# Performance work log

Measured on AMD Instinct MI355X. Metric: run time of the kernel, lower is better.

## Reference

```python
import jax, jax.numpy as jnp
import numpy as np

CH = 50        # channel
RED = 2        # reduction -> match channels = 25
KS = 3         # ksize
SM_SCALE = 10.0
SCALES = [1.0, 0.9, 0.8, 0.7, 0.6]
ESCAPE_NAN = 1e-4


def prelu(x, a):
    return jnp.where(x >= 0, x, a * x)


def conv1x1(x, w, b):
    # x: [B,Ci,H,W], w: [Co,Ci], b: [Co]
    return jnp.einsum('bihw,oi->bohw', x, w) + b[None, :, None, None]


def patches3(x):
    # extract 3x3 stride-1 SAME patches, torch-unfold (C,kh,kw) ordering
    # x: [B,C,H,W] -> [B, H*W, C, 3, 3]
    B, C, H, W = x.shape
    p = jnp.pad(x, ((0, 0), (0, 0), (1, 1), (1, 1)))
    cols = jnp.stack([p[:, :, i:i + H, j:j + W]
                      for i in range(KS) for j in range(KS)], axis=2)  # [B,C,9,H,W]
    cols = cols.reshape(B, C, KS, KS, H * W)
    return cols.transpose(0, 4, 1, 2, 3)


def setup_inputs() -> dict:
    key = jax.random.key(0)
    ks = jax.random.split(key, 7)
    B, H, W = 4, 48, 48
    f = CH // RED  # 25
    s1 = 1.0 / np.sqrt(CH)
    return {
        'x': jax.random.normal(ks[0], (B, CH, H, W), jnp.float32),
        # conv_match_L_base: 1x1 conv CH->f + PReLU
        'w_base': jax.random.normal(ks[1], (f, CH), jnp.float32) * s1,
        'b_base': jnp.zeros((f,), jnp.float32),
        'a_base': jnp.float32(0.25),
        # conv_match: 1x1 conv CH->f + PReLU
        'w_match': jax.random.normal(ks[2], (f, CH), jnp.float32) * s1,
        'b_match': jnp.zeros((f,), jnp.float32),
        'a_match': jnp.float32(0.25),
        # conv_assembly: 1x1 conv CH->CH + PReLU
        'w_asm': jax.random.normal(ks[3], (CH, CH), jnp.float32) * s1,
        'b_asm': jnp.zeros((CH,), jnp.float32),
        'a_asm': jnp.float32(0.25),
    }


def reference(x, w_base, b_base, a_base, w_match, b_match, a_match,
              w_asm, b_asm, a_asm):
    B, C, H, W = x.shape
    match_base = prelu(conv1x1(x, w_base, b_base), a_base)  # [B,25,H,W]

    w_list, raw_list = [], []
    for s in SCALES:
        if s == 1.0:
            ref = x
        else:
            Hs, Ws = int(H * s), int(W * s)
            ref = jax.image.resize(x, (B, C, Hs, Ws), method='cubic')
        base = prelu(conv1x1(ref, w_asm, b_asm), a_asm)       # [B,C,Hs,Ws]
        raw_list.append(patches3(base))                       # [B,Hs*Ws,C,3,3]
        refm = prelu(conv1x1(ref, w_match, b_match), a_match)  # [B,25,Hs,Ws]
        w_list.append(patches3(refm))                         # [B,Hs*Ws,25,3,3]

    wi = jnp.concatenate(w_list, axis=1)    # [B, L, 25, 3, 3]
    raw = jnp.concatenate(raw_list, axis=1)  # [B, L, C, 3, 3]

    def attend(xb, wb, rb):
        # xb: [25,H,W]; wb: [L,25,3,3]; rb: [L,C,3,3]
        norm = jnp.maximum(
            jnp.sqrt(jnp.sum(wb * wb, axis=(1, 2, 3), keepdims=True)),
            ESCAPE_NAN)
        wn = wb / norm
        score = jax.lax.conv_general_dilated(
            xb[None], wn, (1, 1), [(1, 1), (1, 1)])[0]        # [L,H,W]
        attn = jax.nn.softmax(score * SM_SCALE, axis=0)
        # conv_transpose2d(stride=1, pad=1) == corr with flipped, transposed kernel
        wt = jnp.flip(rb, axis=(2, 3)).transpose(1, 0, 2, 3)  # [C,L,3,3]
        out = jax.lax.conv_general_dilated(
            attn[None], wt, (1, 1), [(1, 1), (1, 1)])[0]      # [C,H,W]
        return out * 0.25

    y = jax.vmap(attend)(match_base, wi, raw)
    return y + x  # res_scale = 1
```

## Files before the change

kernel.cpp:

```cpp
#include <hip/hip_runtime.h>
#include <hip/hip_bf16.h>
#include <hip/hip_fp16.h>
#include <math.h>


#define L_TOT 7470
#define L_PAD 7680
#define NCHUNK 4
#define CHUNK_TILES 30
#define KD    256
#define JD    512
#define HW    2304

typedef unsigned short u16;
typedef __attribute__((ext_vector_type(8))) short bf16x8;
typedef __attribute__((ext_vector_type(4))) float f32x4;

__device__ inline u16 f2b(float f) {
    __hip_bfloat16 h = __float2bfloat16(f);
    return __builtin_bit_cast(u16, h);
}
__device__ inline float b2f(u16 u) {
    __hip_bfloat16 h = __builtin_bit_cast(__hip_bfloat16, u);
    return __bfloat162float(h);
}
__device__ inline u16 f2h(float f) {
    __half h = __float2half(f);
    return __builtin_bit_cast(u16, h);
}
__device__ inline float h2f(u16 u) {
    __half h = __builtin_bit_cast(__half, u);
    return __half2float(h);
}

__constant__ int c_hs[5]   = {48, 43, 38, 33, 28};
__constant__ int c_loff[6] = {0, 2304, 4153, 5597, 6686, 7470};

#define GLOAD16(g, l) __builtin_amdgcn_global_load_lds(                          \
        (__attribute__((address_space(1))) const void*)(g),                      \
        (__attribute__((address_space(3))) void*)(l), 16, 0, 0)

__global__ void prep_kernel(float* __restrict__ wmall, int* __restrict__ dtab) {
    int r = blockIdx.x * 256 + threadIdx.x;
    if (r < 142) {
        int sizes[4] = {43, 38, 33, 28};
        int si = 0, i = r, woffs = 0;
        for (si = 0; si < 4; ++si) {
            if (i < sizes[si]) break;
            i -= sizes[si];
            woffs += sizes[si] * 48;
        }
        int osz = sizes[si];
        float inv_scale = 48.0f / (float)osz;
        float kscale = inv_scale;
        float sample_f = ((float)i + 0.5f) * inv_scale - 0.5f;
        float w[48];
        float tot = 0.f;
        for (int j = 0; j < 48; ++j) {
            float t = fabsf(sample_f - (float)j) / kscale;
            float v;
            if (t >= 2.f)       v = 0.f;
            else if (t >= 1.f)  v = ((-0.5f * t + 2.5f) * t - 4.f) * t + 2.f;
            else                v = ((1.5f * t - 2.5f) * t) * t + 1.f;
            w[j] = v;
            tot += v;
        }
        float invt = 1.f / tot;
        for (int j = 0; j < 48; ++j) wmall[woffs + i * 48 + j] = w[j] * invt;
    }
    if (r < L_PAD) {
        int v;
        if (r >= L_TOT) v = (int)0x80000000u;
        else {
            int si = 0;
#pragma unroll
            for (int s = 0; s < 4; ++s)
                if (r >= c_loff[s + 1]) si = s + 1;
            int pos = r - c_loff[si];
            int hs = c_hs[si];
            int ly = pos / hs, lx = pos % hs;
            v = si | (ly << 4) | (lx << 10);
        }
        dtab[r] = v;
    }
}

__global__ void resize_h_all(const float* __restrict__ in, const float* __restrict__ wm,
                             float* __restrict__ t1, float* __restrict__ t2,
                             float* __restrict__ t3, float* __restrict__ t4) {
    int idx = blockIdx.x * 256 + threadIdx.x;
    int rem = idx, osz, woffm;
    float* tmp;
    if (rem < 200 * 43 * 48) { osz = 43; tmp = t1; woffm = 0; }
    else {
        rem -= 200 * 43 * 48;
        if (rem < 200 * 38 * 48) { osz = 38; tmp = t2; woffm = 43 * 48; }
        else {
            rem -= 200 * 38 * 48;
            if (rem < 200 * 33 * 48) { osz = 33; tmp = t3; woffm = (43 + 38) * 48; }
            else {
                rem -= 200 * 33 * 48;
                if (rem >= 200 * 28 * 48) return;
                osz = 28; tmp = t4; woffm = (43 + 38 + 33) * 48;
            }
        }
    }
    int xi = rem % 48;
    int t = rem / 48;
    int yo = t % osz;
    int bc = t / osz;
    const float* wr = wm + (size_t)(woffm + yo * 48);
    const float* ip = in + (size_t)bc * 2304 + xi;
    float s = 0.f;
#pragma unroll
    for (int yi = 0; yi < 48; ++yi) s += wr[yi] * ip[yi * 48];
    tmp[rem] = s;
}

__global__ void resize_w_all(const float* __restrict__ t1, const float* __restrict__ t2,
                             const float* __restrict__ t3, const float* __restrict__ t4,
                             const float* __restrict__ wm,
                             float* __restrict__ r1, float* __restrict__ r2,
                             float* __restrict__ r3, float* __restrict__ r4) {
    int idx = blockIdx.x * 256 + threadIdx.x;
    int rem = idx, osz, woffm;
    const float* tmp;
    float* outp;
    if (rem < 200 * 43 * 43) { osz = 43; tmp = t1; outp = r1; woffm = 0; }
    else {
        rem -= 200 * 43 * 43;
        if (rem < 200 * 38 * 38) { osz = 38; tmp = t2; outp = r2; woffm = 43 * 48; }
        else {
            rem -= 200 * 38 * 38;
            if (rem < 200 * 33 * 33) { osz = 33; tmp = t3; outp = r3; woffm = (43 + 38) * 48; }
            else {
                rem -= 200 * 33 * 33;
                if (rem >= 200 * 28 * 28) return;
                osz = 28; tmp = t4; outp = r4; woffm = (43 + 38 + 33) * 48;
            }
        }
    }
    int xo = rem % osz;
    int t = rem / osz;
    int yo = t % osz;
    int bc = t / osz;
    const float* wr = wm + (size_t)(woffm + xo * 48);
    const float* ip = tmp + ((size_t)bc * osz + yo) * 48;
    float s = 0.f;
#pragma unroll
    for (int xi = 0; xi < 48; ++xi) s += wr[xi] * ip[xi];
    outp[rem] = s;
}

__global__ void conv_all(const float* __restrict__ x,
                         const float* __restrict__ r1, const float* __restrict__ r2,
                         const float* __restrict__ r3, const float* __restrict__ r4,
                         const float* __restrict__ w_asm, const float* __restrict__ b_asm,
                         const float* __restrict__ a_asm,
                         const float* __restrict__ w_match, const float* __restrict__ b_match,
                         const float* __restrict__ a_match,
                         const float* __restrict__ w_base, const float* __restrict__ b_base,
                         const float* __restrict__ a_base,
                         float* __restrict__ base_out, float* __restrict__ refm_out,
                         float* __restrict__ mb_out) {
    int idx = blockIdx.x * 256 + threadIdx.x;
    int rem = idx, P, loffv, NCO;
    const float* in;
    if (rem < 400 * 2304) { P = 2304; in = x; loffv = 0; NCO = 100; }
    else {
        rem -= 400 * 2304;
        if (rem < 300 * 1849) { P = 1849; in = r1; loffv = 2304; NCO = 75; }
        else {
            rem -= 300 * 1849;
            if (rem < 300 * 1444) { P = 1444; in = r2; loffv = 4153; NCO = 75; }
            else {
                rem -= 300 * 1444;
                if (rem < 300 * 1089) { P = 1089; in = r3; loffv = 5597; NCO = 75; }
                else {
                    rem -= 300 * 1089;
                    if (rem >= 300 * 784) return;
                    P = 784; in = r4; loffv = 6686; NCO = 75;
                }
            }
        }
    }
    int p = rem % P;
    int t = rem / P;
    int co = t % NCO;
    int b = t / NCO;
    const float* ip = in + (size_t)b * 50 * P + p;
    const float* wr;
    float bias, av;
    float* outp;
    if (co < 50) {
        wr = w_asm + co * 50; bias = b_asm[co]; av = a_asm[0];
        outp = base_out + (size_t)200 * loffv + ((size_t)(b * 50 + co)) * P + p;
    } else if (co < 75) {
        int cm = co - 50;
        wr = w_match + cm * 50; bias = b_match[cm]; av = a_match[0];
        outp = refm_out + (size_t)100 * loffv + ((size_t)(b * 25 + cm)) * P + p;
    } else {
        int cm = co - 75;
        wr = w_base + cm * 50; bias = b_base[cm]; av = a_base[0];
        outp = mb_out + ((size_t)(b * 25 + cm)) * P + p;
    }
    float s = bias;
#pragma unroll
    for (int ci = 0; ci < 50; ++ci) s += wr[ci] * ip[(size_t)ci * P];
    *outp = (s >= 0.f) ? s : av * s;
}

__global__ void q_build(const float* __restrict__ mb, u16* __restrict__ Q) {
    int idx = blockIdx.x * 256 + threadIdx.x;
    if (idx >= 4 * HW * 25) return;
    int c = idx % 25;
    int t = idx / 25;
    int p = t % HW;
    int b = t / HW;
    int y = p / 48, xx = p % 48;
    const float* rc = mb + (size_t)(b * 25 + c) * HW;
    u16 ov[9];
#pragma unroll
    for (int ky = 0; ky < 3; ++ky)
#pragma unroll
        for (int kx = 0; kx < 3; ++kx) {
            int yy = y + ky - 1, xv = xx + kx - 1;
            float v = (yy >= 0 && yy < 48 && xv >= 0 && xv < 48) ? rc[yy * 48 + xv] : 0.f;
            ov[ky * 3 + kx] = f2b(v);
        }
    u16* dst = Q + (size_t)(b * HW + p) * KD + c * 9;
#pragma unroll
    for (int r = 0; r < 9; ++r) dst[r] = ov[r];
    if (c == 24) {
        u16* z = dst + 9;
#pragma unroll
        for (int i = 0; i < 31; ++i) z[i] = 0;
    }
}

__global__ void norms_kernel(const float* __restrict__ refm_all, const int* __restrict__ dtab,
                             float* __restrict__ norms) {
    int idx = blockIdx.x * 256 + threadIdx.x;
    if (idx >= 4 * L_PAD) return;
    int l = idx % L_PAD;
    int b = idx / L_PAD;
    int d = dtab[l];
    if (d < 0) return;
    int si = d & 15, ly = (d >> 4) & 63, lx = (d >> 10) & 63;
    int hs = c_hs[si], P = hs * hs;
    const float* rb = refm_all + (size_t)100 * c_loff[si] + (size_t)(b * 25) * P;
    float ss = 0.f;
    for (int c = 0; c < 25; ++c) {
        const float* rc = rb + (size_t)c * P;
#pragma unroll
        for (int ky = 0; ky < 3; ++ky)
#pragma unroll
            for (int kx = 0; kx < 3; ++kx) {
                int yy = ly + ky - 1, xv = lx + kx - 1;
                if (yy >= 0 && yy < hs && xv >= 0 && xv < hs) {
                    float v = rc[yy * hs + xv];
                    ss += v * v;
                }
            }
    }
    norms[(size_t)b * L_PAD + l] = 10.0f * 1.44269504f / fmaxf(sqrtf(ss), 1e-4f);
}

__global__ void kt_build(const float* __restrict__ refm_all, const int* __restrict__ dtab,
                         const float* __restrict__ norms, u16* __restrict__ K) {
    int idx = blockIdx.x * 256 + threadIdx.x;
    if (idx >= 4 * L_PAD * 25) return;
    int c = idx % 25;
    int t = idx / 25;
    int l = t % L_PAD;
    int b = t / L_PAD;
    u16 ov[9] = {0, 0, 0, 0, 0, 0, 0, 0, 0};
    int d = dtab[l];
    if (d >= 0) {
        int si = d & 15, ly = (d >> 4) & 63, lx = (d >> 10) & 63;
        int hs = c_hs[si], P = hs * hs;
        float nrm = norms[(size_t)b * L_PAD + l];
        const float* rc = refm_all + (size_t)100 * c_loff[si] + (size_t)(b * 25 + c) * P;
#pragma unroll
        for (int ky = 0; ky < 3; ++ky)
#pragma unroll
            for (int kx = 0; kx < 3; ++kx) {
                int yy = ly + ky - 1, xv = lx + kx - 1;
                if (yy >= 0 && yy < hs && xv >= 0 && xv < hs)
                    ov[ky * 3 + kx] = f2b(rc[yy * hs + xv] * nrm);
            }
    }
    u16* dst = K + (size_t)(b * L_PAD + l) * KD + c * 9;
#pragma unroll
    for (int r = 0; r < 9; ++r) dst[r] = ov[r];
    if (c == 24) {
        u16* z = dst + 9;
#pragma unroll
        for (int i = 0; i < 31; ++i) z[i] = 0;
    }
}

__global__ void v_build(const float* __restrict__ base_all, const int* __restrict__ dtab,
                        u16* __restrict__ VT) {
    int idx = blockIdx.x * 256 + threadIdx.x;
    if (idx >= 4 * JD * (L_PAD / 8)) return;
    int l8 = idx % (L_PAD / 8);
    int t = idx / (L_PAD / 8);
    int j = t % JD;
    int b = t / JD;
    int l0 = l8 * 8;
    bf16x8 ov = (bf16x8){0, 0, 0, 0, 0, 0, 0, 0};
    if (j < 450) {
        int c = j / 9, r = j % 9, ky = r / 3, kx = r % 3;
#pragma unroll
        for (int u = 0; u < 8; ++u) {
            int d = dtab[l0 + u];
            float v = 0.f;
            if (d >= 0) {
                int si = d & 15, ly = (d >> 4) & 63, lx = (d >> 10) & 63;
                int hs = c_hs[si], P = hs * hs;
                int yy = ly + ky - 1, xv = lx + kx - 1;
                if (yy >= 0 && yy < hs && xv >= 0 && xv < hs)
                    v = base_all[(size_t)200 * c_loff[si] + (size_t)(b * 50 + c) * P + yy * hs + xv];
            }
            ov[u] = (short)f2b(v);
        }
    } else if (j == 450) {
        const u16 one = f2b(1.0f);
#pragma unroll
        for (int u = 0; u < 8; ++u)
            ov[u] = (short)(dtab[l0 + u] >= 0 ? one : 0);
    }
    *(bf16x8*)&VT[(size_t)(b * JD + j) * L_PAD + l0] = ov;
}

__global__ __launch_bounds__(256, 4) void attn_score(
    const u16* __restrict__ Qg, const u16* __restrict__ Kg,
    u16* __restrict__ SRg, float* __restrict__ mC) {
    __shared__ u16 smem[64 * KD];
    __shared__ float sm_m[2][32];
    const int bx = blockIdx.x, by = blockIdx.y;
    const int mt = by % 72, zq = by / 72;
    const int z16 = bx + 8 * zq;
    const int b = z16 >> 2, chunk = z16 & 3;
    const int bm = mt * 32;
    const u16* Q = Qg + (size_t)b * HW * KD;
    const u16* K = Kg + (size_t)b * L_PAD * KD;
    u16* SR = SRg + (size_t)b * HW * L_PAD;
    const int tid = threadIdx.x, lane = tid & 63, wid = tid >> 6;
    const int wr = wid >> 1, wc = wid & 1;
    const int l15 = lane & 15, l16 = lane >> 4, l7 = lane & 7;
    const int r_lo = lane >> 5;
    const int u_dst = lane & 31;

    {
        const u16* qrow = Q + (size_t)(bm + wid * 8 + r_lo) * KD;
        u16* qdst = smem + (size_t)(wid * 8) * KD;
#pragma unroll
        for (int q = 0; q < 4; ++q) {
            int sw = (u_dst ^ ((q * 2 + r_lo) & 7)) * 8;
            GLOAD16(qrow + (size_t)(q * 2) * KD + sw, qdst + (q * 2) * KD);
        }
    }
    __syncthreads();
    bf16x8 qf[8];
#pragma unroll
    for (int k = 0; k < 8; ++k)
        qf[k] = *(const bf16x8*)&smem[(size_t)(wr * 16 + l15) * KD + (((k * 4 + l16) ^ l7) * 8)];
    __syncthreads();

    float mrun[4] = {-3e38f, -3e38f, -3e38f, -3e38f};
    const int t0 = chunk * CHUNK_TILES;

    for (int t = t0; t < t0 + CHUNK_TILES; ++t) {
        {
            const u16* krow = K + (size_t)(t * 64 + wid * 16 + r_lo) * KD;
            u16* kdst = smem + (size_t)(wid * 16) * KD;
#pragma unroll
            for (int q = 0; q < 8; ++q) {
                int sw = (u_dst ^ ((q * 2 + r_lo) & 7)) * 8;
                GLOAD16(krow + (size_t)(q * 2) * KD + sw, kdst + (q * 2) * KD);
            }
        }
        __syncthreads();
        f32x4 acc[2];
#pragma unroll
        for (int n = 0; n < 2; ++n) acc[n] = (f32x4){0.f, 0.f, 0.f, 0.f};
#pragma unroll
        for (int k = 0; k < 8; ++k) {
            bf16x8 bfr[2];
#pragma unroll
            for (int n = 0; n < 2; ++n)
                bfr[n] = *(const bf16x8*)&smem[(size_t)(wc * 32 + n * 16 + l15) * KD
                                               + (((k * 4 + l16) ^ l7) * 8)];
#pragma unroll
            for (int n = 0; n < 2; ++n)
                acc[n] = __builtin_amdgcn_mfma_f32_16x16x32_bf16(qf[k], bfr[n], acc[n], 0, 0, 0);
        }
        const int col0 = t * 64 + wc * 32 + l15;
        const int row0 = bm + wr * 16 + l16 * 4;
#pragma unroll
        for (int n = 0; n < 2; ++n) {
            const int col = col0 + n * 16;
            const bool vld = col < L_TOT;
#pragma unroll
            for (int r = 0; r < 4; ++r) {
                float s = acc[n][r];
                if (vld) mrun[r] = fmaxf(mrun[r], s);
                SR[(size_t)(row0 + r) * L_PAD + col] = vld ? f2h(s) : (u16)0xFC00;
            }
        }
        __syncthreads();
    }

#pragma unroll
    for (int r = 0; r < 4; ++r) {
        float mv = mrun[r];
#pragma unroll
        for (int st = 1; st <= 8; st <<= 1)
            mv = fmaxf(mv, __shfl_xor(mv, st));
        mrun[r] = mv;
    }
    if (l15 == 0) {
#pragma unroll
        for (int r = 0; r < 4; ++r)
            sm_m[wc][wr * 16 + l16 * 4 + r] = mrun[r];
    }
    __syncthreads();
    if (wc == 0 && l15 == 0) {
#pragma unroll
        for (int r = 0; r < 4; ++r) {
            int row = wr * 16 + l16 * 4 + r;
            mC[(size_t)(chunk * 4 + b) * HW + bm + row] = fmaxf(sm_m[0][row], sm_m[1][row]);
        }
    }
}

__global__ __launch_bounds__(256) void gemm2_kernel(
    const u16* __restrict__ VT0, const u16* __restrict__ SR0,
    const float* __restrict__ mC, u16* __restrict__ C0) {
    __shared__ u16 As[128 * 64];
    __shared__ u16 Bs[128 * 64];
    const int bx = blockIdx.x, by = blockIdx.y;
    const int within = by % 72, zq = by / 72;
    const int mt = within & 3, nt = within >> 2;
    const int z = bx + 8 * zq;
    const int batch = z >> 2, chunk = z & 3;
    const u16* A = VT0 + (size_t)batch * JD * L_PAD + chunk * (CHUNK_TILES * 64);
    const u16* B = SR0 + (size_t)batch * HW * L_PAD + chunk * (CHUNK_TILES * 64);
    u16* C = C0 + (size_t)z * JD * HW;
    const int bm = mt * 128, bn = nt * 128;
    const int tid = threadIdx.x, lane = tid & 63, wid = tid >> 6;
    const int wr = wid >> 1, wc = wid & 1;
    const int srow = lane >> 3;
    const int u8 = lane & 7;
    const int l15 = lane & 15, l16 = lane >> 4;
    const int swu = (u8 ^ srow) * 8;

    float mrow[4];
    {
        const float* mp = mC + (size_t)(chunk * 4 + batch) * HW;
#pragma unroll
        for (int q = 0; q < 4; ++q)
            mrow[q] = mp[bn + wid * 32 + srow + q * 8];
    }

    f32x4 acc[4][4];
#pragma unroll
    for (int i = 0; i < 4; ++i)
#pragma unroll
        for (int j = 0; j < 4; ++j) acc[i][j] = (f32x4){0.f, 0.f, 0.f, 0.f};

    const u16* aGrow = A + (size_t)(bm + wid * 32 + srow) * L_PAD;
    const u16* bG = B + (size_t)(bn + wid * 32 + srow) * L_PAD + u8 * 8;
    u16* aL = As + wid * 32 * 64;

    union U8 { uint4 v; u16 h[8]; };
    uint4 bv[4];
#pragma unroll
    for (int q = 0; q < 4; ++q)
        bv[q] = *(const uint4*)(bG + (size_t)q * 8 * L_PAD);
    bG += 64;

    for (int t = 0; t < CHUNK_TILES; ++t) {
#pragma unroll
        for (int q = 0; q < 4; ++q)
            GLOAD16(aGrow + (size_t)q * 8 * L_PAD + t * 64 + swu, aL + q * 8 * 64);
        uint4 bnext[4];
        if (t < CHUNK_TILES - 1) {
#pragma unroll
            for (int q = 0; q < 4; ++q)
                bnext[q] = *(const uint4*)(bG + (size_t)q * 8 * L_PAD);
            bG += 64;
        }
#pragma unroll
        for (int q = 0; q < 4; ++q) {
            U8 uu; uu.v = bv[q];
            bf16x8 ob;
#pragma unroll
            for (int u = 0; u < 8; ++u) {
                float e = exp2f(h2f(uu.h[u]) - mrow[q]);
                ob[u] = (short)f2b(e);
            }
            *(bf16x8*)&Bs[(size_t)(wid * 32 + srow + q * 8) * 64 + swu] = ob;
        }
        __syncthreads();
#pragma unroll
        for (int kc = 0; kc < 64; kc += 32) {
            bf16x8 af[4], bf[4];
#pragma unroll
            for (int m = 0; m < 4; ++m)
                af[m] = *(const bf16x8*)&As[(wr * 64 + m * 16 + l15) * 64
                                            + (((kc >> 3) + l16) ^ (l15 & 7)) * 8];
#pragma unroll
            for (int n = 0; n < 4; ++n)
                bf[n] = *(const bf16x8*)&Bs[(wc * 64 + n * 16 + l15) * 64
                                            + (((kc >> 3) + l16) ^ (l15 & 7)) * 8];
#pragma unroll
            for (int m = 0; m < 4; ++m)
#pragma unroll
                for (int n = 0; n < 4; ++n)
                    acc[m][n] = __builtin_amdgcn_mfma_f32_16x16x32_bf16(af[m], bf[n], acc[m][n], 0, 0, 0);
        }
        __syncthreads();
#pragma unroll
        for (int q = 0; q < 4; ++q) bv[q] = bnext[q];
    }
    const int crow0 = bm + wr * 64 + (lane >> 4) * 4;
    const int ccol = bn + wc * 64 + l15;
#pragma unroll
    for (int m = 0; m < 4; ++m)
#pragma unroll
        for (int n = 0; n < 4; ++n)
#pragma unroll
            for (int r = 0; r < 4; ++r)
                C[(size_t)(crow0 + m * 16 + r) * HW + ccol + n * 16] = f2b(acc[m][n][r]);
}

__global__ void combine_stats(const float* __restrict__ mC, const u16* __restrict__ Zt,
                              float* __restrict__ fac) {
    int idx = blockIdx.x * 256 + threadIdx.x;
    if (idx >= 4 * HW) return;
    int b = idx / HW, p = idx % HW;
    float m[NCHUNK], d[NCHUNK];
#pragma unroll
    for (int c = 0; c < NCHUNK; ++c) {
        m[c] = mC[(size_t)(c * 4 + b) * HW + p];
        d[c] = b2f(Zt[((size_t)(b * 4 + c) * JD + 450) * HW + p]);
    }
    float mf = m[0];
#pragma unroll
    for (int c = 1; c < NCHUNK; ++c) mf = fmaxf(mf, m[c]);
    float w[NCHUNK], df = 0.f;
#pragma unroll
    for (int c = 0; c < NCHUNK; ++c) { w[c] = exp2f(m[c] - mf); df += d[c] * w[c]; }
    float inv = 1.0f / df;
#pragma unroll
    for (int c = 0; c < NCHUNK; ++c) fac[(size_t)(c * 4 + b) * HW + p] = w[c] * inv;
}

__global__ void chunk_reduce(const u16* __restrict__ Zt, const float* __restrict__ fac,
                             u16* __restrict__ Zred) {
    int idx = blockIdx.x * 256 + threadIdx.x;
    int total = 4 * JD * HW / 8;
    if (idx >= total) return;
    int e8 = idx * 8;
    int pp = e8 % HW;
    int row = e8 / HW;
    int b = row / JD;
    float s[8] = {};
#pragma unroll
    for (int ch = 0; ch < NCHUNK; ++ch) {
        const float* fp = fac + (size_t)(ch * 4 + b) * HW + pp;
        bf16x8 zv = *(const bf16x8*)&Zt[((size_t)(b * 4 + ch) * JD + (row % JD)) * HW + pp];
#pragma unroll
        for (int u = 0; u < 8; ++u)
            s[u] += fp[u] * b2f((u16)zv[u]);
    }
    bf16x8 o;
#pragma unroll
    for (int u = 0; u < 8; ++u) o[u] = (short)f2b(s[u]);
    *(bf16x8*)&Zred[(size_t)row * HW + pp] = o;
}

__global__ void final_kernel(const u16* __restrict__ Zred, const float* __restrict__ x,
                             float* __restrict__ out) {
    int idx = blockIdx.x * 256 + threadIdx.x;
    if (idx >= 4 * 50 * HW) return;
    int p = idx % HW;
    int t = idx / HW;
    int c = t % 50;
    int b = t / 50;
    int y = p / 48, xx = p % 48;
    const u16* Zb = Zred + (size_t)b * JD * HW;
    float s = 0.f;
#pragma unroll
    for (int ky = 0; ky < 3; ++ky) {
        int yy = y + ky - 1;
        if (yy < 0 || yy >= 48) continue;
#pragma unroll
        for (int kx = 0; kx < 3; ++kx) {
            int xv = xx + kx - 1;
            if (xv < 0 || xv >= 48) continue;
            int pp = yy * 48 + xv;
            int j = c * 9 + (2 - ky) * 3 + (2 - kx);
            s += b2f(Zb[(size_t)j * HW + pp]);
        }
    }
    size_t o = ((size_t)b * 50 + c) * HW + p;
    out[o] = x[o] + 0.25f * s;
}

extern "C" void kernel_launch(void* const* d_in, const int* in_sizes, int n_in,
                              void* d_out, int out_size, void* d_ws, size_t ws_size,
                              hipStream_t stream) {
    const float* x       = (const float*)d_in[0];
    const float* w_base  = (const float*)d_in[1];
    const float* b_base  = (const float*)d_in[2];
    const float* a_base  = (const float*)d_in[3];
    const float* w_match = (const float*)d_in[4];
    const float* b_match = (const float*)d_in[5];
    const float* a_match = (const float*)d_in[6];
    const float* w_asm   = (const float*)d_in[7];
    const float* b_asm   = (const float*)d_in[8];
    const float* a_asm   = (const float*)d_in[9];
    float* out = (float*)d_out;
    float* ws = (float*)d_ws;
    (void)in_sizes; (void)n_in; (void)out_size; (void)ws_size;

    size_t off = 0;
    auto alloc = [&](size_t n) { size_t o = off; off += (n + 63) & ~(size_t)63; return o; };
    size_t o_wm = alloc(142 * 48);
    size_t o_dtab = alloc(L_PAD);
    size_t o_t1 = alloc((size_t)200 * 43 * 48);
    size_t o_t2 = alloc((size_t)200 * 38 * 48);
    size_t o_t3 = alloc((size_t)200 * 33 * 48);
    size_t o_t4 = alloc((size_t)200 * 28 * 48);
    size_t o_r1 = alloc((size_t)200 * 43 * 43);
    size_t o_r2 = alloc((size_t)200 * 38 * 38);
    size_t o_r3 = alloc((size_t)200 * 33 * 33);
    size_t o_r4 = alloc((size_t)200 * 28 * 28);
    size_t o_base = alloc((size_t)200 * L_TOT);
    size_t o_refm = alloc((size_t)100 * L_TOT);
    size_t o_mb = alloc((size_t)100 * HW);
    size_t o_norms = alloc((size_t)4 * L_PAD);

    size_t o_SR = 0;
    size_t o_Q = (size_t)4 * HW * L_PAD / 2;
    size_t o_K = o_Q + (size_t)4 * HW * KD / 2;
    size_t o_VT = o_K + (size_t)4 * L_PAD * KD / 2;
    size_t o_Z = o_VT + (size_t)4 * JD * L_PAD / 2;
    size_t o_mc = o_Z + (size_t)16 * JD * HW / 2;
    size_t o_fac = o_mc + (size_t)16 * HW;
    size_t o_zred = o_fac + (size_t)16 * HW;

    u16* Qb = (u16*)(ws + o_Q);
    u16* Kb = (u16*)(ws + o_K);
    u16* VTb = (u16*)(ws + o_VT);
    u16* SRb = (u16*)(ws + o_SR);
    u16* Zb = (u16*)(ws + o_Z);
    u16* Zrb = (u16*)(ws + o_zred);
    int* dtab = (int*)(ws + o_dtab);

    prep_kernel<<<(L_PAD + 255) / 256, 256, 0, stream>>>(ws + o_wm, dtab);
    {
        int n = 200 * 48 * (43 + 38 + 33 + 28);
        resize_h_all<<<(n + 255) / 256, 256, 0, stream>>>(x, ws + o_wm, ws + o_t1,
                                                          ws + o_t2, ws + o_t3, ws + o_t4);
    }
    {
        int n = 200 * (43 * 43 + 38 * 38 + 33 * 33 + 28 * 28);
        resize_w_all<<<(n + 255) / 256, 256, 0, stream>>>(ws + o_t1, ws + o_t2, ws + o_t3,
                                                          ws + o_t4, ws + o_wm, ws + o_r1,
                                                          ws + o_r2, ws + o_r3, ws + o_r4);
    }
    {
        int n = 400 * 2304 + 300 * (1849 + 1444 + 1089 + 784);
        conv_all<<<(n + 255) / 256, 256, 0, stream>>>(
            x, ws + o_r1, ws + o_r2, ws + o_r3, ws + o_r4,
            w_asm, b_asm, a_asm, w_match, b_match, a_match, w_base, b_base, a_base,
            ws + o_base, ws + o_refm, ws + o_mb);
    }
    {
        int n = 4 * HW * 25;
        q_build<<<(n + 255) / 256, 256, 0, stream>>>(ws + o_mb, Qb);
    }
    {
        int n = 4 * L_PAD;
        norms_kernel<<<(n + 255) / 256, 256, 0, stream>>>(ws + o_refm, dtab, ws + o_norms);
    }
    {
        int n = 4 * L_PAD * 25;
        kt_build<<<(n + 255) / 256, 256, 0, stream>>>(ws + o_refm, dtab, ws + o_norms, Kb);
    }
    {
        int n = 4 * JD * (L_PAD / 8);
        v_build<<<(n + 255) / 256, 256, 0, stream>>>(ws + o_base, dtab, VTb);
    }

    {
        dim3 g(8, 144, 1);
        attn_score<<<g, 256, 0, stream>>>(Qb, Kb, SRb, ws + o_mc);
    }
    {
        dim3 g(8, 144, 1);
        gemm2_kernel<<<g, 256, 0, stream>>>(VTb, SRb, ws + o_mc, Zb);
    }
    combine_stats<<<(4 * HW + 255) / 256, 256, 0, stream>>>(ws + o_mc, Zb, ws + o_fac);
    {
        int n = 4 * JD * HW / 8;
        chunk_reduce<<<(n + 255) / 256, 256, 0, stream>>>(Zb, ws + o_fac, Zrb);
    }
    final_kernel<<<(4 * 50 * HW + 255) / 256, 256, 0, stream>>>(Zrb, x, out);
}
```

Measured before the change: 498.6 us.

## Apply exp normalization in score kernel, load probabilities directly in gemm2

The score kernel now rewrites its own tile of fp16 scores in place as bf16 exponentials, using the per-row chunk max it has just computed. The second GEMM then loads that B operand straight into LDS with async loads, like the A operand, instead of register-staging it and computing exp per tile. Each exponential is now computed once rather than once per output-row tile of gemm2 (4 times). The cost is an extra read-modify-write pass over the score matrix at the end of the score kernel.

```diff
diff --git a/kernel.cpp b/kernel.cpp
--- a/kernel.cpp
+++ b/kernel.cpp
@@ -431,14 +431,33 @@
 #pragma unroll
         for (int r = 0; r < 4; ++r) {
             int row = wr * 16 + l16 * 4 + r;
-            mC[(size_t)(chunk * 4 + b) * HW + bm + row] = fmaxf(sm_m[0][row], sm_m[1][row]);
-        }
+            float mm = fmaxf(sm_m[0][row], sm_m[1][row]);
+            sm_m[0][row] = mm;
+            mC[(size_t)(chunk * 4 + b) * HW + bm + row] = mm;
+        }
+    }
+    __syncthreads();
+
+    const int cb = t0 * 64;
+#pragma unroll 2
+    for (int i = 0; i < 30; ++i) {
+        int id = i * 256 + tid;
+        int row = id / 240;
+        int c8 = id - row * 240;
+        u16* ptr = SR + (size_t)(bm + row) * L_PAD + cb + c8 * 8;
+        float m = sm_m[0][row];
+        bf16x8 iv = *(const bf16x8*)ptr;
+        bf16x8 o;
+#pragma unroll
+        for (int u = 0; u < 8; ++u)
+            o[u] = (short)f2b(exp2f(h2f((u16)iv[u]) - m));
+        *(bf16x8*)ptr = o;
     }
 }
 
 __global__ __launch_bounds__(256) void gemm2_kernel(
-    const u16* __restrict__ VT0, const u16* __restrict__ SR0,
-    const float* __restrict__ mC, u16* __restrict__ C0) {
+    const u16* __restrict__ VT0, const u16* __restrict__ P0,
+    u16* __restrict__ C0) {
     __shared__ u16 As[128 * 64];
     __shared__ u16 Bs[128 * 64];
     const int bx = blockIdx.x, by = blockIdx.y;
@@ -447,7 +466,7 @@
     const int z = bx + 8 * zq;
     const int batch = z >> 2, chunk = z & 3;
     const u16* A = VT0 + (size_t)batch * JD * L_PAD + chunk * (CHUNK_TILES * 64);
-    const u16* B = SR0 + (size_t)batch * HW * L_PAD + chunk * (CHUNK_TILES * 64);
+    const u16* B = P0 + (size_t)batch * HW * L_PAD + chunk * (CHUNK_TILES * 64);
     u16* C = C0 + (size_t)z * JD * HW;
     const int bm = mt * 128, bn = nt * 128;
     const int tid = threadIdx.x, lane = tid & 63, wid = tid >> 6;
@@ -457,14 +476,6 @@
     const int l15 = lane & 15, l16 = lane >> 4;
     const int swu = (u8 ^ srow) * 8;
 
-    float mrow[4];
-    {
-        const float* mp = mC + (size_t)(chunk * 4 + batch) * HW;
-#pragma unroll
-        for (int q = 0; q < 4; ++q)
-            mrow[q] = mp[bn + wid * 32 + srow + q * 8];
-    }
-
     f32x4 acc[4][4];
 #pragma unroll
     for (int i = 0; i < 4; ++i)
@@ -472,50 +483,27 @@
         for (int j = 0; j < 4; ++j) acc[i][j] = (f32x4){0.f, 0.f, 0.f, 0.f};
 
     const u16* aGrow = A + (size_t)(bm + wid * 32 + srow) * L_PAD;
-    const u16* bG = B + (size_t)(bn + wid * 32 + srow) * L_PAD + u8 * 8;
+    const u16* bGrow = B + (size_t)(bn + wid * 32 + srow) * L_PAD;
     u16* aL = As + wid * 32 * 64;
-
-    union U8 { uint4 v; u16 h[8]; };
-    uint4 bv[4];
-#pragma unroll
-    for (int q = 0; q < 4; ++q)
-        bv[q] = *(const uint4*)(bG + (size_t)q * 8 * L_PAD);
-    bG += 64;
+    u16* bL = Bs + wid * 32 * 64;
 
     for (int t = 0; t < CHUNK_TILES; ++t) {
 #pragma unroll
-        for (int q = 0; q < 4; ++q)
+        for (int q = 0; q < 4; ++q) {
             GLOAD16(aGrow + (size_t)q * 8 * L_PAD + t * 64 + swu, aL + q * 8 * 64);
-        uint4 bnext[4];
-        if (t < CHUNK_TILES - 1) {
-#pragma unroll
-            for (int q = 0; q < 4; ++q)
-                bnext[q] = *(const uint4*)(bG + (size_t)q * 8 * L_PAD);
-            bG += 64;
-        }
-#pragma unroll
-        for (int q = 0; q < 4; ++q) {
-            U8 uu; uu.v = bv[q];
-            bf16x8 ob;
-#pragma unroll
-            for (int u = 0; u < 8; ++u) {
-                float e = exp2f(h2f(uu.h[u]) - mrow[q]);
-                ob[u] = (short)f2b(e);
-            }
-            *(bf16x8*)&Bs[(size_t)(wid * 32 + srow + q * 8) * 64 + swu] = ob;
+            GLOAD16(bGrow + (size_t)q * 8 * L_PAD + t * 64 + swu, bL + q * 8 * 64);
         }
         __syncthreads();
 #pragma unroll
         for (int kc = 0; kc < 64; kc += 32) {
+            const int fs = (((kc >> 3) + l16) ^ (l15 & 7)) * 8;
             bf16x8 af[4], bf[4];
 #pragma unroll
             for (int m = 0; m < 4; ++m)
-                af[m] = *(const bf16x8*)&As[(wr * 64 + m * 16 + l15) * 64
-                                            + (((kc >> 3) + l16) ^ (l15 & 7)) * 8];
+                af[m] = *(const bf16x8*)&As[(wr * 64 + m * 16 + l15) * 64 + fs];
 #pragma unroll
             for (int n = 0; n < 4; ++n)
-                bf[n] = *(const bf16x8*)&Bs[(wc * 64 + n * 16 + l15) * 64
-                                            + (((kc >> 3) + l16) ^ (l15 & 7)) * 8];
+                bf[n] = *(const bf16x8*)&Bs[(wc * 64 + n * 16 + l15) * 64 + fs];
 #pragma unroll
             for (int m = 0; m < 4; ++m)
 #pragma unroll
@@ -523,8 +511,6 @@
                     acc[m][n] = __builtin_amdgcn_mfma_f32_16x16x32_bf16(af[m], bf[n], acc[m][n], 0, 0, 0);
         }
         __syncthreads();
-#pragma unroll
-        for (int q = 0; q < 4; ++q) bv[q] = bnext[q];
     }
     const int crow0 = bm + wr * 64 + (lane >> 4) * 4;
     const int ccol = bn + wc * 64 + l15;
@@ -704,7 +690,7 @@
     }
     {
         dim3 g(8, 144, 1);
-        gemm2_kernel<<<g, 256, 0, stream>>>(VTb, SRb, ws + o_mc, Zb);
+        gemm2_kernel<<<g, 256, 0, stream>>>(VTb, SRb, Zb);
     }
     combine_stats<<<(4 * HW + 255) / 256, 256, 0, stream>>>(ws + o_mc, Zb, ws + o_fac);
     {
```

New measurement: 467.0 us. 6.3% less time.
